# Optimization experiments

Measured on AMD Instinct MI355X. Metric: run time of the kernel, lower is better.

The kernel has to match this reference:

```python
import jax, jax.numpy as jnp
import numpy as np

N = 300000  # active lattice vertices
K = 9       # permutohedral 1-ring stencil: center + 2*(d+1) neighbors, d=3
F = 64      # nr_filters


def setup_inputs() -> dict:
    key = jax.random.key(0)
    k1, k2, k3, k4 = jax.random.split(key, 4)
    lv = jax.random.normal(k1, (N, F), dtype=jnp.float32)
    neighbors = jax.random.randint(k2, (N, K), 0, N, dtype=jnp.int64)
    # center tap is the vertex itself (tap 0)
    neighbors = neighbors.at[:, 0].set(jnp.arange(N, dtype=jnp.int64))
    scale = 1.0 / np.sqrt(K * F)
    w1 = jax.random.normal(k3, (K, F, F), dtype=jnp.float32) * scale
    w2 = jax.random.normal(k4, (K, F, F), dtype=jnp.float32) * scale
    b1 = jnp.zeros((F,), dtype=jnp.float32)
    b2 = jnp.zeros((F,), dtype=jnp.float32)
    return {"lv": lv, "neighbors": neighbors, "w1": w1, "b1": b1, "w2": w2, "b2": b2}


def _lattice_conv(x, neighbors, w, b):
    # gather neighbor values: [N, K, F], then per-tap matmul and sum over taps
    g = x[neighbors]  # irregular gather
    return jnp.einsum('nkf,kfo->no', g, w) + b


def reference(lv, neighbors, w1, b1, w2, b2):
    identity = lv
    # ReluConv 1: relu -> lattice conv (dropout disabled)
    x = _lattice_conv(jax.nn.relu(lv), neighbors, w1, b1)
    # ReluConv 2: relu -> lattice conv
    x = _lattice_conv(jax.nn.relu(x), neighbors, w2, b2)
    # residual add
    return x + identity
```

## Files before the change

kernel.cpp:

```cpp
#include <hip/hip_runtime.h>

#define NV 300000
#define KT 9
#define NF 64
#define NBLK ((NV + 63) / 64)

typedef __attribute__((ext_vector_type(8))) short bf16x8;
typedef __attribute__((ext_vector_type(4))) float f32x4;
typedef __attribute__((ext_vector_type(4))) float f4;
typedef __attribute__((ext_vector_type(4))) unsigned short u16x4;

__device__ __forceinline__ unsigned short f2bf(float f) {
    union { float f; unsigned int u; } a; a.f = f;
    unsigned int u = a.u;
    return (unsigned short)((u + 0x7FFFu + ((u >> 16) & 1u)) >> 16);
}

__global__ void prep_kernel(const float* __restrict__ lv,
                            const float* __restrict__ w1,
                            const float* __restrict__ w2,
                            unsigned short* __restrict__ xbf0,
                            unsigned short* __restrict__ wt1,
                            unsigned short* __restrict__ wt2) {
    int b = blockIdx.x;
    if (b < 18) {
        const float* w = (b < 9) ? w1 : w2;
        unsigned short* wt = (b < 9) ? wt1 : wt2;
        int k = (b < 9) ? b : b - 9;
        for (int e = threadIdx.x; e < NF * NF; e += 256) {
            int o = e >> 6, f = e & 63;
            wt[(k * NF + o) * NF + f] = f2bf(w[(k * NF + f) * NF + o]);
        }
    } else {
        const int n4 = NV * NF / 4;
        int i = (b - 18) * 256 + threadIdx.x;
        if (i < n4) {
            f4 v = ((const f4*)lv)[i];
            u16x4 r;
            #pragma unroll
            for (int j = 0; j < 4; ++j) r[j] = f2bf(fmaxf(v[j], 0.f));
            ((u16x4*)xbf0)[i] = r;
        }
    }
}

template<int LAYER>
__global__ __launch_bounds__(256, 8)
void conv_kernel(const unsigned short* __restrict__ xin,
                 const int* __restrict__ nbr,
                 const unsigned short* __restrict__ wt,
                 const float* __restrict__ bias,
                 const float* __restrict__ resid,
                 unsigned short* __restrict__ bfout,
                 float* __restrict__ fout)
{
    __shared__ unsigned short gA[2][64][64];
    __shared__ int nbs[576];

    const int tid  = threadIdx.x;
    const int lane = tid & 63;
    const int wv   = tid >> 6;
    const int base = blockIdx.x * 64;

    for (int e = tid; e < 576; e += 256) {
        long ge = (long)base * 9 + e;
        nbs[e] = (ge < (long)NV * 9) ? nbr[ge] : 0;
    }

    const int bcol = wv * 16 + (lane & 15);
    const int bk   = (lane >> 4) * 8;
    auto ldw = [&](int k, int kk) {
        return *(const bf16x8*)&wt[(k * 64 + bcol) * 64 + kk * 32 + bk];
    };

    f32x4 acc[4];
    #pragma unroll
    for (int im = 0; im < 4; ++im) acc[im] = (f32x4){0.f, 0.f, 0.f, 0.f};

    __syncthreads();

    const int sr_off = lane >> 3;
    const int sj     = lane & 7;
    auto stage = [&](int k) {
        #pragma unroll
        for (int h = 0; h < 2; ++h) {
            const int rblk = wv + h * 4;
            const int r    = rblk * 8 + sr_off;
            const int nb   = nbs[r * 9 + k];
            const int gcol = sj ^ (r & 7);
            const unsigned short* src = xin + nb * 64 + gcol * 8;
            __builtin_amdgcn_global_load_lds(
                (const __attribute__((address_space(1))) unsigned int*)src,
                (__attribute__((address_space(3))) unsigned int*)&gA[k & 1][rblk * 8][0],
                16, 0, 0);
        }
    };

    auto tap = [&](int k, bf16x8 (&bwk)[2]) {
        #pragma unroll
        for (int im = 0; im < 4; ++im) {
            #pragma unroll
            for (int kk = 0; kk < 2; ++kk) {
                const int row = im * 16 + (lane & 15);
                const int c16 = kk * 4 + (lane >> 4);
                const int swc = c16 ^ (row & 7);
                bf16x8 a = *(const bf16x8*)&gA[k & 1][row][swc * 8];
                acc[im] = __builtin_amdgcn_mfma_f32_16x16x32_bf16(a, bwk[kk], acc[im], 0, 0, 0);
            }
        }
    };

    #define FENCE asm volatile("" ::: "memory")

    bf16x8 bwreg[2][2];

    bwreg[0][0] = ldw(0, 0); bwreg[0][1] = ldw(0, 1); stage(0); FENCE;
    bwreg[1][0] = ldw(1, 0); bwreg[1][1] = ldw(1, 1); stage(1); FENCE;

    #define PHASE(K, VM)                                                   \
        asm volatile("s_waitcnt vmcnt(" #VM ")" ::: "memory");             \
        __builtin_amdgcn_s_barrier();                                      \
        tap(K, bwreg[(K) & 1]);                                            \
        FENCE;                                                             \
        __builtin_amdgcn_s_barrier();                                      \
        if ((K) + 2 <= 8) {                                                \
            stage((K) + 2);                                                \
            bwreg[(K) & 1][0] = ldw((K) + 2, 0);                           \
            bwreg[(K) & 1][1] = ldw((K) + 2, 1);                           \
        }                                                                  \
        FENCE;
    PHASE(0, 4) PHASE(1, 4) PHASE(2, 4) PHASE(3, 4) PHASE(4, 4)
    PHASE(5, 4) PHASE(6, 4) PHASE(7, 4) PHASE(8, 0)
    #undef PHASE
    #undef FENCE

    const int ocol = wv * 16 + (lane & 15);
    const int orow = (lane >> 4) * 4;
    const float bv = bias[ocol];
    #pragma unroll
    for (int im = 0; im < 4; ++im) {
        #pragma unroll
        for (int j = 0; j < 4; ++j) {
            const int r = base + im * 16 + orow + j;
            if (r < NV) {
                float v = acc[im][j] + bv;
                if (LAYER == 1) {
                    bfout[r * 64 + ocol] = f2bf(fmaxf(v, 0.f));
                } else {
                    fout[r * 64 + ocol] = v + resid[r * 64 + ocol];
                }
            }
        }
    }
}

extern "C" void kernel_launch(void* const* d_in, const int* in_sizes, int n_in,
                              void* d_out, int out_size, void* d_ws, size_t ws_size,
                              hipStream_t stream) {
    const float* lv  = (const float*)d_in[0];
    const int*   nbr = (const int*)d_in[1];
    const float* w1  = (const float*)d_in[2];
    const float* b1  = (const float*)d_in[3];
    const float* w2  = (const float*)d_in[4];
    const float* b2  = (const float*)d_in[5];
    float* out = (float*)d_out;

    char* ws = (char*)d_ws;
    unsigned short* xbf0 = (unsigned short*)ws;
    unsigned short* xbf1 = (unsigned short*)(ws + 38400000);
    unsigned short* wt1  = (unsigned short*)(ws + 76800000);
    unsigned short* wt2  = (unsigned short*)(ws + 76873728);

    const int n4blk = (NV * NF / 4 + 255) / 256;
    prep_kernel<<<18 + n4blk, 256, 0, stream>>>(lv, w1, w2, xbf0, wt1, wt2);
    conv_kernel<1><<<NBLK, 256, 0, stream>>>(xbf0, nbr, wt1, b1, nullptr, xbf1, nullptr);
    conv_kernel<2><<<NBLK, 256, 0, stream>>>(xbf1, nbr, wt2, b2, lv, nullptr, out);
}
```

Before: 282.3 us.

## Make each wave own its 16 rows to drop block-wide barriers in conv

Each wave now gathers and computes its own 16 rows against all 64 output columns, so the LDS tile is private to the wave and the per-tap s_barrier pairs are removed. Weights for all four column blocks are loaded per tap instead of being double-buffered in registers, and staging now prefetches only one tap ahead. This removes block-level synchronisation stalls in exchange for four times the weight loads per wave, more live registers, and a shallower prefetch.

```diff
diff --git a/kernel.cpp b/kernel.cpp
--- a/kernel.cpp
+++ b/kernel.cpp
@@ -54,7 +54,7 @@
                  unsigned short* __restrict__ bfout,
                  float* __restrict__ fout)
 {
-    __shared__ unsigned short gA[2][64][64];
+    __shared__ unsigned short gA[2][4][16][64];
     __shared__ int nbs[576];
 
     const int tid  = threadIdx.x;
@@ -67,87 +67,87 @@
         nbs[e] = (ge < (long)NV * 9) ? nbr[ge] : 0;
     }
 
-    const int bcol = wv * 16 + (lane & 15);
-    const int bk   = (lane >> 4) * 8;
-    auto ldw = [&](int k, int kk) {
-        return *(const bf16x8*)&wt[(k * 64 + bcol) * 64 + kk * 32 + bk];
-    };
+    float bv[4];
+    #pragma unroll
+    for (int n = 0; n < 4; ++n) bv[n] = bias[n * 16 + (lane & 15)];
 
     f32x4 acc[4];
     #pragma unroll
-    for (int im = 0; im < 4; ++im) acc[im] = (f32x4){0.f, 0.f, 0.f, 0.f};
+    for (int n = 0; n < 4; ++n) acc[n] = (f32x4){0.f, 0.f, 0.f, 0.f};
 
     __syncthreads();
 
-    const int sr_off = lane >> 3;
-    const int sj     = lane & 7;
+    const int srow = lane >> 3;
+    const int sj   = lane & 7;
     auto stage = [&](int k) {
         #pragma unroll
         for (int h = 0; h < 2; ++h) {
-            const int rblk = wv + h * 4;
-            const int r    = rblk * 8 + sr_off;
-            const int nb   = nbs[r * 9 + k];
-            const int gcol = sj ^ (r & 7);
+            const int row16 = h * 8 + srow;
+            const int nb    = nbs[(wv * 16 + row16) * 9 + k];
+            const int gcol  = sj ^ (row16 & 7);
             const unsigned short* src = xin + nb * 64 + gcol * 8;
             __builtin_amdgcn_global_load_lds(
                 (const __attribute__((address_space(1))) unsigned int*)src,
-                (__attribute__((address_space(3))) unsigned int*)&gA[k & 1][rblk * 8][0],
+                (__attribute__((address_space(3))) unsigned int*)&gA[k & 1][wv][h * 8][0],
                 16, 0, 0);
         }
     };
 
-    auto tap = [&](int k, bf16x8 (&bwk)[2]) {
+    auto ldw = [&](int k, int n, int kk) {
+        return *(const bf16x8*)&wt[(k * 64 + n * 16 + (lane & 15)) * 64 + kk * 32 + (lane >> 4) * 8];
+    };
+
+    auto tap = [&](int k, bf16x8 (&bwk)[4][2]) {
         #pragma unroll
-        for (int im = 0; im < 4; ++im) {
+        for (int n = 0; n < 4; ++n) {
             #pragma unroll
             for (int kk = 0; kk < 2; ++kk) {
-                const int row = im * 16 + (lane & 15);
+                const int row = lane & 15;
                 const int c16 = kk * 4 + (lane >> 4);
                 const int swc = c16 ^ (row & 7);
-                bf16x8 a = *(const bf16x8*)&gA[k & 1][row][swc * 8];
-                acc[im] = __builtin_amdgcn_mfma_f32_16x16x32_bf16(a, bwk[kk], acc[im], 0, 0, 0);
+                bf16x8 a = *(const bf16x8*)&gA[k & 1][wv][row][swc * 8];
+                acc[n] = __builtin_amdgcn_mfma_f32_16x16x32_bf16(a, bwk[n][kk], acc[n], 0, 0, 0);
             }
         }
     };
 
     #define FENCE asm volatile("" ::: "memory")
 
-    bf16x8 bwreg[2][2];
-
-    bwreg[0][0] = ldw(0, 0); bwreg[0][1] = ldw(0, 1); stage(0); FENCE;
-    bwreg[1][0] = ldw(1, 0); bwreg[1][1] = ldw(1, 1); stage(1); FENCE;
+    stage(0); FENCE;
 
     #define PHASE(K, VM)                                                   \
+    {                                                                      \
+        bf16x8 bwk[4][2];                                                  \
+        _Pragma("unroll")                                                  \
+        for (int n = 0; n < 4; ++n) {                                      \
+            bwk[n][0] = ldw(K, n, 0);                                      \
+            bwk[n][1] = ldw(K, n, 1);                                      \
+        }                                                                  \
+        FENCE;                                                             \
+        if ((K) < 8) stage((K) + 1);                                       \
+        FENCE;                                                             \
         asm volatile("s_waitcnt vmcnt(" #VM ")" ::: "memory");             \
-        __builtin_amdgcn_s_barrier();                                      \
-        tap(K, bwreg[(K) & 1]);                                            \
+        tap(K, bwk);                                                       \
         FENCE;                                                             \
-        __builtin_amdgcn_s_barrier();                                      \
-        if ((K) + 2 <= 8) {                                                \
-            stage((K) + 2);                                                \
-            bwreg[(K) & 1][0] = ldw((K) + 2, 0);                           \
-            bwreg[(K) & 1][1] = ldw((K) + 2, 1);                           \
-        }                                                                  \
-        FENCE;
-    PHASE(0, 4) PHASE(1, 4) PHASE(2, 4) PHASE(3, 4) PHASE(4, 4)
-    PHASE(5, 4) PHASE(6, 4) PHASE(7, 4) PHASE(8, 0)
+    }
+    PHASE(0, 2) PHASE(1, 2) PHASE(2, 2) PHASE(3, 2) PHASE(4, 2)
+    PHASE(5, 2) PHASE(6, 2) PHASE(7, 2) PHASE(8, 0)
     #undef PHASE
     #undef FENCE
 
-    const int ocol = wv * 16 + (lane & 15);
-    const int orow = (lane >> 4) * 4;
-    const float bv = bias[ocol];
+    const int orow = base + wv * 16 + (lane >> 4) * 4;
     #pragma unroll
-    for (int im = 0; im < 4; ++im) {
+    for (int n = 0; n < 4; ++n) {
+        const int c = n * 16 + (lane & 15);
         #pragma unroll
         for (int j = 0; j < 4; ++j) {
-            const int r = base + im * 16 + orow + j;
+            const int r = orow + j;
             if (r < NV) {
-                float v = acc[im][j] + bv;
+                float v = acc[n][j] + bv[n];
                 if (LAYER == 1) {
-                    bfout[r * 64 + ocol] = f2bf(fmaxf(v, 0.f));
+                    bfout[r * 64 + c] = f2bf(fmaxf(v, 0.f));
                 } else {
-                    fout[r * 64 + ocol] = v + resid[r * 64 + ocol];
+                    fout[r * 64 + c] = v + resid[r * 64 + c];
                 }
             }
         }
```

Result: slower. 489.8 us (+73.5%).
